# Kernel tuning notes

Measured on AMD Instinct MI355X. Metric: run time of the kernel, lower is better.

The kernel has to match this reference:

```python
import jax, jax.numpy as jnp
import numpy as np

LRELU = 0.2
EPS_LN = 1e-5
EPS_BN = 1e-5


def _seg_softmax(logits, seg, n):
    # softmax over edges grouped by destination node (PyG softmax), logits [E,H]
    m = jax.ops.segment_max(logits, seg, num_segments=n)
    e = jnp.exp(logits - m[seg])
    s = jax.ops.segment_sum(e, seg, num_segments=n)
    return e / (s[seg] + 1e-16)


def _gat(x, src, dst, n, W, a_src, a_dst, b, H, C):
    # PyG GATConv, concat=False (mean over heads), leaky_relu slope 0.2
    h = (x @ W).reshape(n, H, C)
    e = (h * a_src).sum(-1)[src] + (h * a_dst).sum(-1)[dst]  # [E,H]
    e = jnp.where(e > 0, e, LRELU * e)
    alpha = _seg_softmax(e, dst, n)
    out = jax.ops.segment_sum(h[src] * alpha[:, :, None], dst, num_segments=n)  # [N,H,C]
    return out.mean(1) + b


def _gcn(x, src, dst, n, W, b):
    # PyG GCNConv with symmetric normalization; edge list already contains self loops
    deg = jax.ops.segment_sum(jnp.ones(src.shape, x.dtype), dst, num_segments=n)
    dis = jnp.where(deg > 0, jax.lax.rsqrt(jnp.maximum(deg, 1e-12)), 0.0)
    h = x @ W
    w = (dis[src] * dis[dst])[:, None]
    return jax.ops.segment_sum(h[src] * w, dst, num_segments=n) + b


def _ln(x, g, b):
    mu = x.mean(-1, keepdims=True)
    v = x.var(-1, keepdims=True)
    return (x - mu) * jax.lax.rsqrt(v + EPS_LN) * g + b


def _bn_eval(x, g, b, rm, rv):
    return (x - rm) * jax.lax.rsqrt(rv + EPS_BN) * g + b


def _forward(x, edge_index, gin, bti, rmi, rvi, W1, as1, ad1, b1, Wg1, bg1,
             W2, as2, ad2, b2, Wg2, bg2, Ws, bs, Wf, bf,
             g1, be1, g2, be2, g3, be3, Wc1, bc1, gbn, bbn, rmb, rvb, Wc2, bc2):
    n = x.shape[0]
    xn = _bn_eval(x, gin, bti, rmi, rvi)
    sl = jnp.arange(n, dtype=edge_index.dtype)
    src = jnp.concatenate([edge_index[0], sl])
    dst = jnp.concatenate([edge_index[1], sl])
    # GAT1 (4 heads, 128) -> LN -> relu
    x1 = _gat(xn, src, dst, n, W1, as1, ad1, b1, 4, 128)
    x1 = jax.nn.relu(_ln(x1, g1, be1))
    # GCN1 -> relu
    x1g = jax.nn.relu(_gcn(x1, src, dst, n, Wg1, bg1))
    # GAT2 (2 heads, 64) -> LN -> relu
    x2 = _gat(x1g, src, dst, n, W2, as2, ad2, b2, 2, 64)
    x2 = jax.nn.relu(_ln(x2, g2, be2))
    # GCN2 -> relu
    x2g = jax.nn.relu(_gcn(x2, src, dst, n, Wg2, bg2))
    # skip + fusion
    skip = jax.nn.relu(xn @ Ws + bs)
    fused = jax.nn.relu(jnp.concatenate([x1g, x2g], axis=1) @ Wf + bf)
    final = _ln(fused + skip, g3, be3)
    # classifier: Linear -> BN(eval) -> relu -> Linear
    h = jax.nn.relu(_bn_eval(final @ Wc1 + bc1, gbn, bbn, rmb, rvb))
    return h @ Wc2 + bc2


def setup_inputs():
    key = jax.random.key(0)
    ks = jax.random.split(key, 20)
    N, F, E = 20000, 512, 160000
    H1, C1, H2, C2 = 4, 128, 2, 64
    rn = lambda k, sh, s=0.05: (jax.random.normal(k, sh) * s).astype(jnp.float32)
    return dict(
        x=jax.random.normal(ks[0], (N, F), jnp.float32),
        edge_index=jax.random.randint(ks[1], (2, E), 0, N, jnp.int32),
        gin=jnp.ones((F,), jnp.float32), bti=jnp.zeros((F,), jnp.float32),
        rmi=rn(ks[2], (F,)), rvi=(jax.random.uniform(ks[3], (F,)) + 0.5).astype(jnp.float32),
        W1=rn(ks[4], (F, H1 * C1)), as1=rn(ks[5], (H1, C1)), ad1=rn(ks[6], (H1, C1)), b1=jnp.zeros((C1,), jnp.float32),
        Wg1=rn(ks[7], (C1, C1)), bg1=jnp.zeros((C1,), jnp.float32),
        W2=rn(ks[8], (C1, H2 * C2)), as2=rn(ks[9], (H2, C2)), ad2=rn(ks[10], (H2, C2)), b2=jnp.zeros((C2,), jnp.float32),
        Wg2=rn(ks[11], (C2, C2)), bg2=jnp.zeros((C2,), jnp.float32),
        Ws=rn(ks[12], (F, C2)), bs=jnp.zeros((C2,), jnp.float32),
        Wf=rn(ks[13], (C1 + C2, C2)), bf=jnp.zeros((C2,), jnp.float32),
        g1=jnp.ones((C1,), jnp.float32), be1=jnp.zeros((C1,), jnp.float32),
        g2=jnp.ones((C2,), jnp.float32), be2=jnp.zeros((C2,), jnp.float32),
        g3=jnp.ones((C2,), jnp.float32), be3=jnp.zeros((C2,), jnp.float32),
        Wc1=rn(ks[14], (C2, 32)), bc1=jnp.zeros((32,), jnp.float32),
        gbn=jnp.ones((32,), jnp.float32), bbn=jnp.zeros((32,), jnp.float32),
        rmb=rn(ks[15], (32,)), rvb=(jax.random.uniform(ks[16], (32,)) + 0.5).astype(jnp.float32),
        Wc2=rn(ks[17], (32, 5)), bc2=jnp.zeros((5,), jnp.float32),
    )


def reference(x, edge_index, gin, bti, rmi, rvi, W1, as1, ad1, b1, Wg1, bg1,
              W2, as2, ad2, b2, Wg2, bg2, Ws, bs, Wf, bf,
              g1, be1, g2, be2, g3, be3, Wc1, bc1, gbn, bbn, rmb, rvb, Wc2, bc2):
    return _forward(x, edge_index, gin, bti, rmi, rvi, W1, as1, ad1, b1, Wg1, bg1,
                    W2, as2, ad2, b2, Wg2, bg2, Ws, bs, Wf, bf,
                    g1, be1, g2, be2, g3, be3, Wc1, bc1, gbn, bbn, rmb, rvb, Wc2, bc2)
```

## Files before the change

### kernel.cpp

```cpp
#include <hip/hip_runtime.h>
#include <hip/hip_bf16.h>

#define N_NODES 20000
#define F_IN 512

typedef __attribute__((ext_vector_type(8))) short short8;
typedef __attribute__((ext_vector_type(4))) float f32x4;

__device__ __forceinline__ ushort f2bf(float f) {
    uint u = __float_as_uint(f);
    u += 0x7FFF + ((u >> 16) & 1);
    return (ushort)(u >> 16);
}
__device__ __forceinline__ float bf2f(ushort h) { return __uint_as_float((uint)h << 16); }

__device__ __forceinline__ void gload_lds16(const void* g, void* l) {
    __builtin_amdgcn_global_load_lds(
        (const __attribute__((address_space(1))) void*)g,
        (__attribute__((address_space(3))) void*)l, 16, 0, 0);
}

__device__ __forceinline__ f32x4 shfl_xor4(f32x4 v, int m) {
    f32x4 r;
#pragma unroll
    for (int i = 0; i < 4; i++) r[i] = __shfl_xor(v[i], m);
    return r;
}

__global__ void zero_int_k(int* p, int n) {
    int i = blockIdx.x * blockDim.x + threadIdx.x;
    if (i < n) p[i] = 0;
}

__global__ void hist_k(const int* __restrict__ ei, int E0, int N, int* __restrict__ deg) {
    int e = blockIdx.x * blockDim.x + threadIdx.x;
    int Etot = E0 + N;
    if (e >= Etot) return;
    int dst = (e < E0) ? ei[E0 + e] : (e - E0);
    atomicAdd(&deg[dst], 1);
}

__global__ __launch_bounds__(1024) void scan_k(const int* __restrict__ deg, int* __restrict__ rp,
                                               int* __restrict__ fp, float* __restrict__ dis,
                                               int N, int Etot) {
    __shared__ int part[1024];
    int tid = threadIdx.x;
    int chunk = (N + 1023) / 1024;
    int lo = tid * chunk, hi = min(lo + chunk, N);
    int s = 0;
    for (int i = lo; i < hi; i++) s += deg[i];
    part[tid] = s;
    __syncthreads();
    for (int off = 1; off < 1024; off <<= 1) {
        int t = 0;
        if (tid >= off) t = part[tid - off];
        __syncthreads();
        part[tid] += t;
        __syncthreads();
    }
    int run = part[tid] - s;
    for (int i = lo; i < hi; i++) {
        rp[i] = run; fp[i] = run;
        int d = deg[i];
        dis[i] = (d > 0) ? rsqrtf((float)d) : 0.f;
        run += d;
    }
    if (tid == 1023) { rp[N] = Etot; fp[N] = Etot; }
}

__global__ void scatter_k(const int* __restrict__ ei, int E0, int N, int* __restrict__ fp,
                          int* __restrict__ csr_src) {
    int e = blockIdx.x * blockDim.x + threadIdx.x;
    int Etot = E0 + N;
    if (e >= Etot) return;
    int src, dst;
    if (e < E0) { src = ei[e]; dst = ei[E0 + e]; }
    else        { src = e - E0; dst = src; }
    int pos = atomicAdd(&fp[dst], 1);
    csr_src[pos] = src;
}

__global__ void bnprep_k(const float* __restrict__ g, const float* __restrict__ b,
                         const float* __restrict__ rm, const float* __restrict__ rv,
                         float* __restrict__ sc, float* __restrict__ sh, int n) {
    int i = blockIdx.x * blockDim.x + threadIdx.x;
    if (i >= n) return;
    float s = g[i] * rsqrtf(rv[i] + 1e-5f);
    sc[i] = s;
    sh[i] = b[i] - rm[i] * s;
}

__global__ void splitA_k(const float* __restrict__ x, const float* __restrict__ sc,
                         const float* __restrict__ sh, ushort* __restrict__ Ah,
                         ushort* __restrict__ Al, int M, int Mpad) {
    size_t i4 = (size_t)blockIdx.x * blockDim.x + threadIdx.x;
    size_t base = i4 * 4;
    if (base >= (size_t)Mpad * 512) return;
    int row = (int)(base >> 9);
    ushort4 ah = {0, 0, 0, 0}, al = {0, 0, 0, 0};
    if (row < M) {
        float4 v = *(const float4*)&x[base];
        int c = (int)(base & 511);
        float f0 = v.x * sc[c] + sh[c];
        float f1 = v.y * sc[c + 1] + sh[c + 1];
        float f2 = v.z * sc[c + 2] + sh[c + 2];
        float f3 = v.w * sc[c + 3] + sh[c + 3];
        ah.x = f2bf(f0); al.x = f2bf(f0 - bf2f(ah.x));
        ah.y = f2bf(f1); al.y = f2bf(f1 - bf2f(ah.y));
        ah.z = f2bf(f2); al.z = f2bf(f2 - bf2f(ah.z));
        ah.w = f2bf(f3); al.w = f2bf(f3 - bf2f(ah.w));
    }
    *(ushort4*)&Ah[base] = ah;
    *(ushort4*)&Al[base] = al;
}

__global__ __launch_bounds__(256) void splitBt_k(const float* __restrict__ W1, const float* __restrict__ Ws,
                                                 ushort* __restrict__ Bth, ushort* __restrict__ Btl) {
    __shared__ float tile[64][65];
    int n0 = blockIdx.x * 64;
    int k0 = blockIdx.y * 64;
    int t = threadIdx.x;
    int a = t >> 6, b = t & 63;
#pragma unroll
    for (int i = 0; i < 16; i++) {
        int kk = a + i * 4, nn = b;
        int gk = k0 + kk, gn = n0 + nn;
        float v;
        if (gn < 512)      v = W1[(size_t)gk * 512 + gn];
        else if (gn < 576) v = Ws[(size_t)gk * 64 + (gn - 512)];
        else               v = 0.f;
        tile[kk][nn] = v;
    }
    __syncthreads();
#pragma unroll
    for (int i = 0; i < 16; i++) {
        int nn = a + i * 4, kk = b;
        float v = tile[kk][nn];
        ushort hi = f2bf(v);
        ushort lo = f2bf(v - bf2f(hi));
        Bth[(size_t)(n0 + nn) * 512 + k0 + kk] = hi;
        Btl[(size_t)(n0 + nn) * 512 + k0 + kk] = lo;
    }
}

__global__ __launch_bounds__(256) void mfma_gemm_k(
    const ushort* __restrict__ Ah, const ushort* __restrict__ Al,
    const ushort* __restrict__ Bth, const ushort* __restrict__ Btl,
    const float* __restrict__ bs, const float* __restrict__ as1, const float* __restrict__ ad1,
    float* __restrict__ h1, float* __restrict__ skip,
    float* __restrict__ ss1, float* __restrict__ sd1,
    int M, int K) {
    __shared__ ushort A_s[128 * 64];
    __shared__ ushort B_s[128 * 64];
    __shared__ float s1buf[128], s2buf[128];
    int t = threadIdx.x;
    int w = t >> 6, l = t & 63;

    int nwg = gridDim.x;
    int q = nwg >> 3, r = nwg & 7;
    int xcd = blockIdx.x & 7, lid = blockIdx.x >> 3;
    int wg = (xcd < r) ? xcd * (q + 1) + lid : r * (q + 1) + (xcd - r) * q + lid;
    int by = wg / 5, bx = wg % 5;
    int bm = by * 128;
    int n0 = bx * 128;
    int r0 = (w & 1) * 64, c0 = (w >> 1) * 64;

    f32x4 acc[4][4] = {};

    int sl = (t & 7) ^ ((t >> 3) & 7);
    const ushort* aArr = (sl < 4) ? Ah : Al;
    const ushort* bArr = (sl < 4) ? Bth : Btl;
    int ko = (sl & 3) * 8;
    size_t asrc[4], bsrc[4];
#pragma unroll
    for (int c = 0; c < 4; c++) {
        int rr = c * 32 + (t >> 3);
        asrc[c] = (size_t)(bm + rr) * 512 + ko;
        bsrc[c] = (size_t)(n0 + rr) * 512 + ko;
    }
    int d0 = t * 8;

    for (int kt = 0; kt < K; kt += 32) {
#pragma unroll
        for (int c = 0; c < 4; c++) gload_lds16(aArr + asrc[c] + kt, &A_s[c * 2048 + d0]);
#pragma unroll
        for (int c = 0; c < 4; c++) gload_lds16(bArr + bsrc[c] + kt, &B_s[c * 2048 + d0]);
        __syncthreads();

        short8 ah[4], al4[4], bh[4], bl[4];
        int lr = l & 15, kg = l >> 4;
        int spa = kg ^ (lr & 7);
#pragma unroll
        for (int f = 0; f < 4; f++) {
            int ra = (r0 + f * 16 + lr) * 64;
            ah[f]  = *(const short8*)&A_s[ra + spa * 8];
            al4[f] = *(const short8*)&A_s[ra + (spa ^ 4) * 8];
            int rb = (c0 + f * 16 + lr) * 64;
            bh[f] = *(const short8*)&B_s[rb + spa * 8];
            bl[f] = *(const short8*)&B_s[rb + (spa ^ 4) * 8];
        }
#pragma unroll
        for (int fm = 0; fm < 4; fm++)
#pragma unroll
            for (int fn = 0; fn < 4; fn++) {
                acc[fm][fn] = __builtin_amdgcn_mfma_f32_16x16x32_bf16(ah[fm], bh[fn], acc[fm][fn], 0, 0, 0);
                acc[fm][fn] = __builtin_amdgcn_mfma_f32_16x16x32_bf16(ah[fm], bl[fn], acc[fm][fn], 0, 0, 0);
                acc[fm][fn] = __builtin_amdgcn_mfma_f32_16x16x32_bf16(al4[fm], bh[fn], acc[fm][fn], 0, 0, 0);
            }
        __syncthreads();
    }

    int lr = l & 15, kg = l >> 4;
#pragma unroll
    for (int fm = 0; fm < 4; fm++) {
        int row_base = bm + r0 + fm * 16 + kg * 4;
#pragma unroll
        for (int fn = 0; fn < 4; fn++) {
            int col = n0 + c0 + fn * 16 + lr;
#pragma unroll
            for (int r2 = 0; r2 < 4; r2++) {
                int row = row_base + r2;
                if (row < M) {
                    float v = acc[fm][fn][r2];
                    if (col < 512) h1[(size_t)row * 512 + col] = v;
                    else if (col < 576) skip[(size_t)row * 64 + (col - 512)] = fmaxf(v + bs[col - 512], 0.f);
                }
            }
        }
    }

    if (t < 128) { s1buf[t] = 0.f; s2buf[t] = 0.f; }
    __syncthreads();
    if (bx < 4) {
        float aw_[4], dw_[4];
#pragma unroll
        for (int fn = 0; fn < 4; fn++) {
            int col = n0 + c0 + fn * 16 + lr;
            aw_[fn] = as1[col];
            dw_[fn] = ad1[col];
        }
#pragma unroll
        for (int fm = 0; fm < 4; fm++)
#pragma unroll
            for (int r2 = 0; r2 < 4; r2++) {
                float p1 = acc[fm][0][r2] * aw_[0] + acc[fm][1][r2] * aw_[1] +
                           acc[fm][2][r2] * aw_[2] + acc[fm][3][r2] * aw_[3];
                float p2 = acc[fm][0][r2] * dw_[0] + acc[fm][1][r2] * dw_[1] +
                           acc[fm][2][r2] * dw_[2] + acc[fm][3][r2] * dw_[3];
#pragma unroll
                for (int off = 1; off < 16; off <<= 1) {
                    p1 += __shfl_xor(p1, off);
                    p2 += __shfl_xor(p2, off);
                }
                if (lr == 0) {
                    int rloc = r0 + fm * 16 + kg * 4 + r2;
                    atomicAdd(&s1buf[rloc], p1);
                    atomicAdd(&s2buf[rloc], p2);
                }
            }
    }
    __syncthreads();
    if (bx < 4 && t < 128 && bm + t < M) {
        ss1[(size_t)(bm + t) * 4 + bx] = s1buf[t];
        sd1[(size_t)(bm + t) * 4 + bx] = s2buf[t];
    }
}

template <int K, int NOUT, bool SC>
__global__ __launch_bounds__(NOUT) void rowgemm_k(const float* __restrict__ X, const float* __restrict__ W,
                                                  float* __restrict__ out,
                                                  const float* __restrict__ a_src, const float* __restrict__ a_dst,
                                                  float* __restrict__ ss, float* __restrict__ sd, int N) {
    __shared__ float Ws[K * NOUT];
    __shared__ float Xs[8][K];
    int c = threadIdx.x;
    for (int i = c; i < K * NOUT; i += NOUT) Ws[i] = W[i];
    float asv = 0.f, adv = 0.f;
    if (SC) { asv = a_src[c]; adv = a_dst[c]; }
    for (int r0 = blockIdx.x * 8; r0 < N; r0 += gridDim.x * 8) {
        int nr = min(8, N - r0);
        __syncthreads();
        for (int i = c; i < nr * K; i += NOUT) Xs[i / K][i % K] = X[(size_t)r0 * K + i];
        __syncthreads();
        float acc[8] = {};
        for (int k = 0; k < K; k++) {
            float w = Ws[k * NOUT + c];
#pragma unroll
            for (int r = 0; r < 8; r++) acc[r] += Xs[r][k] * w;
        }
        for (int r = 0; r < nr; r++) out[(size_t)(r0 + r) * NOUT + c] = acc[r];
        if (SC) {
            int head = c >> 6;
            for (int r = 0; r < nr; r++) {
                float p1 = acc[r] * asv, p2 = acc[r] * adv;
#pragma unroll
                for (int off = 1; off < 64; off <<= 1) {
                    p1 += __shfl_xor(p1, off);
                    p2 += __shfl_xor(p2, off);
                }
                if ((c & 63) == 0) {
                    ss[(size_t)(r0 + r) * 2 + head] = p1;
                    sd[(size_t)(r0 + r) * 2 + head] = p2;
                }
            }
        }
    }
}

template <int H, int C>
__global__ __launch_bounds__(C) void gat_agg_k(const float* __restrict__ h, const float* __restrict__ ss,
                                               const float* __restrict__ sd, const float* __restrict__ bias,
                                               const float* __restrict__ g, const float* __restrict__ be,
                                               const int* __restrict__ rp, const int* __restrict__ csr_src,
                                               float* __restrict__ out, int N) {
    int n = blockIdx.x;
    int tid = threadIdx.x;
    __shared__ float m_s[H], s_s[H];
    __shared__ __align__(16) float red4[32][4];
    __shared__ int srcs[64];
    __shared__ float aw[64 * H];
    int e0 = rp[n], deg = rp[n + 1] - e0;
    bool small = (deg <= 64);
    int hh = tid >> 5, l = tid & 31;

    if (small && tid < deg) srcs[tid] = csr_src[e0 + tid];
    __syncthreads();

    float sdv = sd[n * H + hh];
    float m = -1e30f, s = 0.f;
    for (int k = l; k < deg; k += 32) {
        int src = small ? srcs[k] : csr_src[e0 + k];
        float e = ss[src * H + hh] + sdv;
        e = (e > 0.f) ? e : 0.2f * e;
        if (small) aw[k * H + hh] = e;
        float mn = fmaxf(m, e);
        s = s * __expf(m - mn) + __expf(e - mn);
        m = mn;
    }
#pragma unroll
    for (int off = 16; off; off >>= 1) {
        float mo = __shfl_xor(m, off), so = __shfl_xor(s, off);
        float mn = fmaxf(m, mo);
        s = s * __expf(m - mn) + so * __expf(mo - mn);
        m = mn;
    }
    if (l == 0) { m_s[hh] = m; s_s[hh] = s + 1e-16f; }
    __syncthreads();

    constexpr int LPR = H * C / 4;
    constexpr int EIF = C / LPR;
    int ep = tid / LPR;
    int o  = (tid % LPR) * 4;
    int hq = o / C;
    f32x4 acc = {0.f, 0.f, 0.f, 0.f};

    if (small) {
        for (int idx = tid; idx < deg * H; idx += C) {
            int h2 = idx & (H - 1);
            aw[idx] = __expf(aw[idx] - m_s[h2]) / s_s[h2];
        }
        __syncthreads();
        for (int k = 0; k < deg; k += EIF) {
            int e = k + ep;
            if (EIF == 1 || e < deg) {
                f32x4 v = *(const f32x4*)(h + (size_t)srcs[e] * (H * C) + o);
                acc += aw[e * H + hq] * v;
            }
        }
    } else {
        for (int t0 = 0; t0 < deg; t0 += 64) {
            int tl = min(64, deg - t0);
            __syncthreads();
            if (tid < tl) srcs[tid] = csr_src[e0 + t0 + tid];
            __syncthreads();
            for (int idx = tid; idx < tl * H; idx += C) {
                int k = idx / H, h2 = idx & (H - 1);
                float e = ss[srcs[k] * H + h2] + sd[n * H + h2];
                e = (e > 0.f) ? e : 0.2f * e;
                aw[idx] = __expf(e - m_s[h2]) / s_s[h2];
            }
            __syncthreads();
            for (int k = 0; k < tl; k += EIF) {
                int e = k + ep;
                if (EIF == 1 || e < tl) {
                    f32x4 v = *(const f32x4*)(h + (size_t)srcs[e] * (H * C) + o);
                    acc += aw[e * H + hq] * v;
                }
            }
        }
    }

    if (H == 4) {
        acc += shfl_xor4(acc, 32);
        if (tid >= 64 && (tid & 63) < 32) *(f32x4*)&red4[tid & 31][0] = acc;
        __syncthreads();
        if (tid < 32) {
            f32x4 o2 = *(const f32x4*)&red4[tid][0];
            acc += o2;
            f32x4 b4 = *(const f32x4*)&bias[tid * 4];
            f32x4 v4 = acc * 0.25f + b4;
            float s1 = v4[0] + v4[1] + v4[2] + v4[3];
#pragma unroll
            for (int off = 1; off < 32; off <<= 1) s1 += __shfl_xor(s1, off);
            float mu = s1 * (1.f / C);
            f32x4 d4 = v4 - mu;
            float s2 = d4[0]*d4[0] + d4[1]*d4[1] + d4[2]*d4[2] + d4[3]*d4[3];
#pragma unroll
            for (int off = 1; off < 32; off <<= 1) s2 += __shfl_xor(s2, off);
            float rs = rsqrtf(s2 * (1.f / C) + 1e-5f);
            f32x4 g4 = *(const f32x4*)&g[tid * 4];
            f32x4 e4 = *(const f32x4*)&be[tid * 4];
            f32x4 y;
#pragma unroll
            for (int i = 0; i < 4; i++) y[i] = fmaxf(d4[i] * rs * g4[i] + e4[i], 0.f);
            *(f32x4*)(out + (size_t)n * C + tid * 4) = y;
        }
    } else {
        acc += shfl_xor4(acc, 32);
        acc += shfl_xor4(acc, 16);
        if (tid < 16) {
            f32x4 b4 = *(const f32x4*)&bias[tid * 4];
            f32x4 v4 = acc * 0.5f + b4;
            float s1 = v4[0] + v4[1] + v4[2] + v4[3];
#pragma unroll
            for (int off = 1; off < 16; off <<= 1) s1 += __shfl_xor(s1, off);
            float mu = s1 * (1.f / C);
            f32x4 d4 = v4 - mu;
            float s2 = d4[0]*d4[0] + d4[1]*d4[1] + d4[2]*d4[2] + d4[3]*d4[3];
#pragma unroll
            for (int off = 1; off < 16; off <<= 1) s2 += __shfl_xor(s2, off);
            float rs = rsqrtf(s2 * (1.f / C) + 1e-5f);
            f32x4 g4 = *(const f32x4*)&g[tid * 4];
            f32x4 e4 = *(const f32x4*)&be[tid * 4];
            f32x4 y;
#pragma unroll
            for (int i = 0; i < 4; i++) y[i] = fmaxf(d4[i] * rs * g4[i] + e4[i], 0.f);
            *(f32x4*)(out + (size_t)n * C + tid * 4) = y;
        }
    }
}

__global__ __launch_bounds__(128) void gcn_agg128_k(const float* __restrict__ h, const float* __restrict__ dis,
                                                    const float* __restrict__ bias, const int* __restrict__ rp,
                                                    const int* __restrict__ csr_src, float* __restrict__ out, int N) {
    int n = blockIdx.x;
    int tid = threadIdx.x;
    __shared__ int srcs[64];
    __shared__ float w[64];
    __shared__ __align__(16) float red4[32][4];
    int e0 = rp[n], deg = rp[n + 1] - e0;
    float dn = dis[n];
    int ep = tid >> 5;
    int c0 = (tid & 31) * 4;
    f32x4 acc = {0.f, 0.f, 0.f, 0.f};
    for (int t0 = 0; t0 < deg; t0 += 64) {
        int tl = min(64, deg - t0);
        if (tid < tl) {
            int s = csr_src[e0 + t0 + tid];
            srcs[tid] = s;
            w[tid] = dis[s] * dn;
        }
        __syncthreads();
        for (int k = 0; k < tl; k += 4) {
            int e = k + ep;
            if (e < tl) {
                f32x4 v = *(const f32x4*)(h + (size_t)srcs[e] * 128 + c0);
                acc += w[e] * v;
            }
        }
        __syncthreads();
    }
    acc += shfl_xor4(acc, 32);
    if (tid >= 64 && (tid & 63) < 32) *(f32x4*)&red4[tid & 31][0] = acc;
    __syncthreads();
    if (tid < 32) {
        f32x4 o2 = *(const f32x4*)&red4[tid][0];
        acc += o2;
        f32x4 b4 = *(const f32x4*)&bias[c0];
        f32x4 y;
#pragma unroll
        for (int i = 0; i < 4; i++) y[i] = fmaxf(acc[i] + b4[i], 0.f);
        *(f32x4*)(out + (size_t)n * 128 + c0) = y;
    }
}

__global__ __launch_bounds__(256) void final_fused_k(
    const float* __restrict__ hg2, const float* __restrict__ dis, const float* __restrict__ bg2,
    const int* __restrict__ rp, const int* __restrict__ csr_src,
    const float* __restrict__ x1g, const float* __restrict__ Wf, const float* __restrict__ bf,
    const float* __restrict__ skip, const float* __restrict__ g3, const float* __restrict__ be3,
    const float* __restrict__ Wc1, const float* __restrict__ bc1, const float* __restrict__ gbn,
    const float* __restrict__ bbn, const float* __restrict__ rmb, const float* __restrict__ rvb,
    const float* __restrict__ Wc2, const float* __restrict__ bc2, float* __restrict__ out, int N) {
    int wv = threadIdx.x >> 6;
    int t  = threadIdx.x & 63;
    int n = blockIdx.x * 4 + wv;
    __shared__ __align__(16) float cat_s[4][192];
    __shared__ float fbuf_s[4][64];
    __shared__ float hbuf_s[4][32];
    if (n >= N) return;

    int e0 = rp[n], deg = rp[n + 1] - e0;
    float dn = dis[n];
    int ep = t >> 4;
    int o = (t & 15) * 4;
    f32x4 acc = {0.f, 0.f, 0.f, 0.f};
    for (int k = 0; k < deg; k += 4) {
        int e = k + ep;
        if (e < deg) {
            int s = csr_src[e0 + e];
            f32x4 v = *(const f32x4*)(hg2 + (size_t)s * 64 + o);
            acc += (dis[s] * dn) * v;
        }
    }
    acc += shfl_xor4(acc, 32);
    acc += shfl_xor4(acc, 16);
    if (t < 16) {
        f32x4 b4 = *(const f32x4*)&bg2[t * 4];
        f32x4 xv;
#pragma unroll
        for (int i = 0; i < 4; i++) xv[i] = fmaxf(acc[i] + b4[i], 0.f);
        *(f32x4*)&cat_s[wv][128 + t * 4] = xv;
    }
    if (t < 32) *(f32x4*)&cat_s[wv][t * 4] = *(const f32x4*)(x1g + (size_t)n * 128 + t * 4);
    float fa = bf[t];
    const float* cat = cat_s[wv];
    for (int j = 0; j < 192; j++) fa += cat[j] * Wf[j * 64 + t];
    fa = fmaxf(fa, 0.f) + skip[(size_t)n * 64 + t];
    float t1 = fa;
#pragma unroll
    for (int off = 1; off < 64; off <<= 1) t1 += __shfl_xor(t1, off);
    float mu = t1 * (1.f / 64.f);
    float d = fa - mu;
    float t2 = d * d;
#pragma unroll
    for (int off = 1; off < 64; off <<= 1) t2 += __shfl_xor(t2, off);
    float var = t2 * (1.f / 64.f);
    fbuf_s[wv][t] = d * rsqrtf(var + 1e-5f) * g3[t] + be3[t];
    if (t < 32) {
        float a = bc1[t];
        for (int j = 0; j < 64; j++) a += fbuf_s[wv][j] * Wc1[j * 32 + t];
        a = (a - rmb[t]) * rsqrtf(rvb[t] + 1e-5f) * gbn[t] + bbn[t];
        hbuf_s[wv][t] = fmaxf(a, 0.f);
    }
    if (t < 5) {
        float a = bc2[t];
        for (int j = 0; j < 32; j++) a += hbuf_s[wv][j] * Wc2[j * 5 + t];
        out[(size_t)n * 5 + t] = a;
    }
}

extern "C" void kernel_launch(void* const* d_in, const int* in_sizes, int n_in,
                              void* d_out, int out_size, void* d_ws, size_t ws_size,
                              hipStream_t stream) {
    const float* x   = (const float*)d_in[0];
    const int*   ei  = (const int*)d_in[1];
    const float* gin = (const float*)d_in[2];
    const float* bti = (const float*)d_in[3];
    const float* rmi = (const float*)d_in[4];
    const float* rvi = (const float*)d_in[5];
    const float* W1  = (const float*)d_in[6];
    const float* as1 = (const float*)d_in[7];
    const float* ad1 = (const float*)d_in[8];
    const float* b1  = (const float*)d_in[9];
    const float* Wg1 = (const float*)d_in[10];
    const float* bg1 = (const float*)d_in[11];
    const float* W2  = (const float*)d_in[12];
    const float* as2 = (const float*)d_in[13];
    const float* ad2 = (const float*)d_in[14];
    const float* b2  = (const float*)d_in[15];
    const float* Wg2 = (const float*)d_in[16];
    const float* bg2 = (const float*)d_in[17];
    const float* Ws  = (const float*)d_in[18];
    const float* bs  = (const float*)d_in[19];
    const float* Wf  = (const float*)d_in[20];
    const float* bf  = (const float*)d_in[21];
    const float* g1  = (const float*)d_in[22];
    const float* be1 = (const float*)d_in[23];
    const float* g2  = (const float*)d_in[24];
    const float* be2 = (const float*)d_in[25];
    const float* g3  = (const float*)d_in[26];
    const float* be3 = (const float*)d_in[27];
    const float* Wc1 = (const float*)d_in[28];
    const float* bc1 = (const float*)d_in[29];
    const float* gbn = (const float*)d_in[30];
    const float* bbn = (const float*)d_in[31];
    const float* rmb = (const float*)d_in[32];
    const float* rvb = (const float*)d_in[33];
    const float* Wc2 = (const float*)d_in[34];
    const float* bc2 = (const float*)d_in[35];
    float* out = (float*)d_out;

    const int N = in_sizes[0] / F_IN;
    const int E0 = in_sizes[1] / 2;
    const int Etot = E0 + N;
    const int Mpad = 20096;

    char* wp = (char*)d_ws;
    auto alloc = [&](size_t bytes) -> void* {
        void* p = (void*)wp;
        wp += (bytes + 255) & ~(size_t)255;
        return p;
    };
    float* h1   = (float*)alloc((size_t)N * 512 * 4);
    ushort* Ah  = (ushort*)alloc((size_t)Mpad * 512 * 2);
    ushort* Al  = (ushort*)alloc((size_t)Mpad * 512 * 2);
    ushort* Bth = (ushort*)alloc((size_t)640 * 512 * 2);
    ushort* Btl = (ushort*)alloc((size_t)640 * 512 * 2);
    float* skip = (float*)alloc((size_t)N * 64 * 4);
    float* ss1  = (float*)alloc((size_t)N * 4 * 4);
    float* sd1  = (float*)alloc((size_t)N * 4 * 4);
    float* ss2  = (float*)alloc((size_t)N * 2 * 4);
    float* sd2  = (float*)alloc((size_t)N * 2 * 4);
    float* dis  = (float*)alloc((size_t)N * 4);
    float* sc   = (float*)alloc((size_t)F_IN * 4);
    float* sh   = (float*)alloc((size_t)F_IN * 4);
    int* deg    = (int*)alloc((size_t)N * 4);
    int* rp     = (int*)alloc((size_t)(N + 1) * 4);
    int* fp     = (int*)alloc((size_t)(N + 1) * 4);
    int* csr    = (int*)alloc((size_t)Etot * 4);
    float* hg1 = h1;
    float* x1g = h1 + (size_t)N * 128;
    float* h2  = h1 + (size_t)N * 256;
    float* x2  = h1 + (size_t)N * 384;
    float* hg2 = h1 + (size_t)N * 448;
    float* x1  = (float*)Ah;

    zero_int_k<<<(N + 255) / 256, 256, 0, stream>>>(deg, N);
    hist_k<<<(Etot + 255) / 256, 256, 0, stream>>>(ei, E0, N, deg);
    scan_k<<<1, 1024, 0, stream>>>(deg, rp, fp, dis, N, Etot);
    scatter_k<<<(Etot + 255) / 256, 256, 0, stream>>>(ei, E0, N, fp, csr);
    bnprep_k<<<2, 256, 0, stream>>>(gin, bti, rmi, rvi, sc, sh, F_IN);
    splitA_k<<<(int)(((size_t)Mpad * 512 / 4 + 255) / 256), 256, 0, stream>>>(x, sc, sh, Ah, Al, N, Mpad);
    splitBt_k<<<dim3(10, 8), 256, 0, stream>>>(W1, Ws, Bth, Btl);

    mfma_gemm_k<<<785, 256, 0, stream>>>(Ah, Al, Bth, Btl, bs, as1, ad1, h1, skip, ss1, sd1, N, 512);

    gat_agg_k<4, 128><<<N, 128, 0, stream>>>(h1, ss1, sd1, b1, g1, be1, rp, csr, x1, N);

    rowgemm_k<128, 128, false><<<1280, 128, 0, stream>>>(x1, Wg1, hg1, nullptr, nullptr, nullptr, nullptr, N);
    gcn_agg128_k<<<N, 128, 0, stream>>>(hg1, dis, bg1, rp, csr, x1g, N);

    rowgemm_k<128, 128, true><<<1280, 128, 0, stream>>>(x1g, W2, h2, as2, ad2, ss2, sd2, N);
    gat_agg_k<2, 64><<<N, 64, 0, stream>>>(h2, ss2, sd2, b2, g2, be2, rp, csr, x2, N);

    rowgemm_k<64, 64, false><<<1280, 64, 0, stream>>>(x2, Wg2, hg2, nullptr, nullptr, nullptr, nullptr, N);

    final_fused_k<<<(N + 3) / 4, 256, 0, stream>>>(hg2, dis, bg2, rp, csr, x1g, Wf, bf, skip, g3, be3,
                                                   Wc1, bc1, gbn, bbn, rmb, rvb, Wc2, bc2, out, N);
}
```

Baseline: 555.5 us.

## Fuse graph aggregation stages with following dense GEMMs into per-tile kernels

Replaces the separate GAT aggregation, GCN aggregation and row-GEMM kernels with three fused kernels. Each block aggregates 8 nodes (one wave per two nodes) into shared memory and then multiplies them by the next layer's weight matrix. This removes the global round-trips and launches for the intermediate x1/x2 activations. Weights are now read from global/L2 per block rather than staged in LDS. GAT1 aggregation processes one node per wave with per-edge recompute of alpha instead of block-wide edge staging.

```diff
diff --git a/kernel.cpp b/kernel.cpp
--- a/kernel.cpp
+++ b/kernel.cpp
@@ -266,221 +266,246 @@
     }
 }
 
-template <int K, int NOUT, bool SC>
-__global__ __launch_bounds__(NOUT) void rowgemm_k(const float* __restrict__ X, const float* __restrict__ W,
-                                                  float* __restrict__ out,
-                                                  const float* __restrict__ a_src, const float* __restrict__ a_dst,
-                                                  float* __restrict__ ss, float* __restrict__ sd, int N) {
-    __shared__ float Ws[K * NOUT];
-    __shared__ float Xs[8][K];
-    int c = threadIdx.x;
-    for (int i = c; i < K * NOUT; i += NOUT) Ws[i] = W[i];
-    float asv = 0.f, adv = 0.f;
-    if (SC) { asv = a_src[c]; adv = a_dst[c]; }
-    for (int r0 = blockIdx.x * 8; r0 < N; r0 += gridDim.x * 8) {
-        int nr = min(8, N - r0);
-        __syncthreads();
-        for (int i = c; i < nr * K; i += NOUT) Xs[i / K][i % K] = X[(size_t)r0 * K + i];
-        __syncthreads();
-        float acc[8] = {};
-        for (int k = 0; k < K; k++) {
-            float w = Ws[k * NOUT + c];
-#pragma unroll
-            for (int r = 0; r < 8; r++) acc[r] += Xs[r][k] * w;
-        }
-        for (int r = 0; r < nr; r++) out[(size_t)(r0 + r) * NOUT + c] = acc[r];
-        if (SC) {
-            int head = c >> 6;
-            for (int r = 0; r < nr; r++) {
-                float p1 = acc[r] * asv, p2 = acc[r] * adv;
-#pragma unroll
-                for (int off = 1; off < 64; off <<= 1) {
-                    p1 += __shfl_xor(p1, off);
-                    p2 += __shfl_xor(p2, off);
+__global__ __launch_bounds__(256) void gat1_gcn1_k(
+    const float* __restrict__ h1, const float* __restrict__ ss1, const float* __restrict__ sd1,
+    const float* __restrict__ b1, const float* __restrict__ g1, const float* __restrict__ be1,
+    const int* __restrict__ rp, const int* __restrict__ csr,
+    const float* __restrict__ Wg1, float* __restrict__ hg1, int N) {
+    __shared__ __align__(16) float x1s[8][128];
+    int t = threadIdx.x;
+    int l = t & 63, wv = t >> 6;
+    int hh = l >> 4, lr = l & 15;
+
+    for (int i = 0; i < 2; i++) {
+        int nl = wv * 2 + i;
+        int n = blockIdx.x * 8 + nl;
+        if (n < N) {
+            int e0 = rp[n], deg = rp[n + 1] - e0;
+            float sdv = sd1[n * 4 + hh];
+            float m = -1e30f, s = 0.f;
+            for (int k = lr; k < deg; k += 16) {
+                int src = csr[e0 + k];
+                float e = ss1[src * 4 + hh] + sdv;
+                e = (e > 0.f) ? e : 0.2f * e;
+                float mn = fmaxf(m, e);
+                s = s * __expf(m - mn) + __expf(e - mn);
+                m = mn;
+            }
+#pragma unroll
+            for (int off = 8; off; off >>= 1) {
+                float mo = __shfl_xor(m, off), so = __shfl_xor(s, off);
+                float mn = fmaxf(m, mo);
+                s = s * __expf(m - mn) + so * __expf(mo - mn);
+                m = mn;
+            }
+            s += 1e-16f;
+            f32x4 a0 = {0, 0, 0, 0}, a1 = {0, 0, 0, 0};
+            for (int k = 0; k < deg; k++) {
+                int src = csr[e0 + k];
+                float e = ss1[src * 4 + hh] + sdv;
+                e = (e > 0.f) ? e : 0.2f * e;
+                float al = __expf(e - m) / s;
+                const float* hp = h1 + (size_t)src * 512 + hh * 128 + lr * 8;
+                a0 += al * *(const f32x4*)hp;
+                a1 += al * *(const f32x4*)(hp + 4);
+            }
+            a0 += shfl_xor4(a0, 16); a1 += shfl_xor4(a1, 16);
+            a0 += shfl_xor4(a0, 32); a1 += shfl_xor4(a1, 32);
+            f32x4 v0 = a0 * 0.25f + *(const f32x4*)&b1[lr * 8];
+            f32x4 v1 = a1 * 0.25f + *(const f32x4*)&b1[lr * 8 + 4];
+            float s1 = v0[0] + v0[1] + v0[2] + v0[3] + v1[0] + v1[1] + v1[2] + v1[3];
+#pragma unroll
+            for (int off = 8; off; off >>= 1) s1 += __shfl_xor(s1, off);
+            float mu = s1 * (1.f / 128.f);
+            f32x4 d0 = v0 - mu, d1 = v1 - mu;
+            float s2 = d0[0]*d0[0] + d0[1]*d0[1] + d0[2]*d0[2] + d0[3]*d0[3] +
+                       d1[0]*d1[0] + d1[1]*d1[1] + d1[2]*d1[2] + d1[3]*d1[3];
+#pragma unroll
+            for (int off = 8; off; off >>= 1) s2 += __shfl_xor(s2, off);
+            float rs = rsqrtf(s2 * (1.f / 128.f) + 1e-5f);
+            if (l < 16) {
+                f32x4 g4a = *(const f32x4*)&g1[lr * 8], g4b = *(const f32x4*)&g1[lr * 8 + 4];
+                f32x4 e4a = *(const f32x4*)&be1[lr * 8], e4b = *(const f32x4*)&be1[lr * 8 + 4];
+                f32x4 y0, y1;
+#pragma unroll
+                for (int j = 0; j < 4; j++) {
+                    y0[j] = fmaxf(d0[j] * rs * g4a[j] + e4a[j], 0.f);
+                    y1[j] = fmaxf(d1[j] * rs * g4b[j] + e4b[j], 0.f);
                 }
-                if ((c & 63) == 0) {
-                    ss[(size_t)(r0 + r) * 2 + head] = p1;
-                    sd[(size_t)(r0 + r) * 2 + head] = p2;
-                }
-            }
-        }
-    }
-}
-
-template <int H, int C>
-__global__ __launch_bounds__(C) void gat_agg_k(const float* __restrict__ h, const float* __restrict__ ss,
-                                               const float* __restrict__ sd, const float* __restrict__ bias,
-                                               const float* __restrict__ g, const float* __restrict__ be,
-                                               const int* __restrict__ rp, const int* __restrict__ csr_src,
-                                               float* __restrict__ out, int N) {
-    int n = blockIdx.x;
-    int tid = threadIdx.x;
-    __shared__ float m_s[H], s_s[H];
-    __shared__ __align__(16) float red4[32][4];
-    __shared__ int srcs[64];
-    __shared__ float aw[64 * H];
-    int e0 = rp[n], deg = rp[n + 1] - e0;
-    bool small = (deg <= 64);
-    int hh = tid >> 5, l = tid & 31;
-
-    if (small && tid < deg) srcs[tid] = csr_src[e0 + tid];
+                *(f32x4*)&x1s[nl][lr * 8] = y0;
+                *(f32x4*)&x1s[nl][lr * 8 + 4] = y1;
+            }
+        }
+    }
     __syncthreads();
 
-    float sdv = sd[n * H + hh];
-    float m = -1e30f, s = 0.f;
-    for (int k = l; k < deg; k += 32) {
-        int src = small ? srcs[k] : csr_src[e0 + k];
-        float e = ss[src * H + hh] + sdv;
-        e = (e > 0.f) ? e : 0.2f * e;
-        if (small) aw[k * H + hh] = e;
-        float mn = fmaxf(m, e);
-        s = s * __expf(m - mn) + __expf(e - mn);
-        m = mn;
-    }
-#pragma unroll
-    for (int off = 16; off; off >>= 1) {
-        float mo = __shfl_xor(m, off), so = __shfl_xor(s, off);
-        float mn = fmaxf(m, mo);
-        s = s * __expf(m - mn) + so * __expf(mo - mn);
-        m = mn;
-    }
-    if (l == 0) { m_s[hh] = m; s_s[hh] = s + 1e-16f; }
+    int c = t & 127, rh = t >> 7;
+    float acc[4] = {};
+    for (int k = 0; k < 128; k += 4) {
+        float w0 = Wg1[(size_t)k * 128 + c];
+        float w1 = Wg1[(size_t)(k + 1) * 128 + c];
+        float w2 = Wg1[(size_t)(k + 2) * 128 + c];
+        float w3 = Wg1[(size_t)(k + 3) * 128 + c];
+#pragma unroll
+        for (int r = 0; r < 4; r++) {
+            f32x4 xv = *(const f32x4*)&x1s[rh * 4 + r][k];
+            acc[r] += xv[0] * w0 + xv[1] * w1 + xv[2] * w2 + xv[3] * w3;
+        }
+    }
+    for (int r = 0; r < 4; r++) {
+        int n = blockIdx.x * 8 + rh * 4 + r;
+        if (n < N) hg1[(size_t)n * 128 + c] = acc[r];
+    }
+}
+
+__global__ __launch_bounds__(256) void gcn1_gat2gemm_k(
+    const float* __restrict__ hg1, const float* __restrict__ dis, const float* __restrict__ bg1,
+    const int* __restrict__ rp, const int* __restrict__ csr,
+    const float* __restrict__ W2, const float* __restrict__ as2, const float* __restrict__ ad2,
+    float* __restrict__ x1g, float* __restrict__ h2,
+    float* __restrict__ ss2, float* __restrict__ sd2, int N) {
+    __shared__ __align__(16) float xs[8][128];
+    int t = threadIdx.x;
+    int l = t & 63, wv = t >> 6;
+    int ep = l >> 5, c4 = (l & 31) * 4;
+
+    for (int i = 0; i < 2; i++) {
+        int nl = wv * 2 + i;
+        int n = blockIdx.x * 8 + nl;
+        if (n < N) {
+            int e0 = rp[n], deg = rp[n + 1] - e0;
+            float dn = dis[n];
+            f32x4 acc = {0, 0, 0, 0};
+            for (int k = ep; k < deg; k += 2) {
+                int src = csr[e0 + k];
+                acc += (dis[src] * dn) * *(const f32x4*)(hg1 + (size_t)src * 128 + c4);
+            }
+            acc += shfl_xor4(acc, 32);
+            if (l < 32) {
+                f32x4 b4 = *(const f32x4*)&bg1[c4];
+                f32x4 y;
+#pragma unroll
+                for (int j = 0; j < 4; j++) y[j] = fmaxf(acc[j] + b4[j], 0.f);
+                *(f32x4*)&xs[nl][c4] = y;
+                *(f32x4*)(x1g + (size_t)n * 128 + c4) = y;
+            }
+        }
+    }
     __syncthreads();
 
-    constexpr int LPR = H * C / 4;
-    constexpr int EIF = C / LPR;
-    int ep = tid / LPR;
-    int o  = (tid % LPR) * 4;
-    int hq = o / C;
-    f32x4 acc = {0.f, 0.f, 0.f, 0.f};
-
-    if (small) {
-        for (int idx = tid; idx < deg * H; idx += C) {
-            int h2 = idx & (H - 1);
-            aw[idx] = __expf(aw[idx] - m_s[h2]) / s_s[h2];
-        }
-        __syncthreads();
-        for (int k = 0; k < deg; k += EIF) {
-            int e = k + ep;
-            if (EIF == 1 || e < deg) {
-                f32x4 v = *(const f32x4*)(h + (size_t)srcs[e] * (H * C) + o);
-                acc += aw[e * H + hq] * v;
-            }
-        }
-    } else {
-        for (int t0 = 0; t0 < deg; t0 += 64) {
-            int tl = min(64, deg - t0);
-            __syncthreads();
-            if (tid < tl) srcs[tid] = csr_src[e0 + t0 + tid];
-            __syncthreads();
-            for (int idx = tid; idx < tl * H; idx += C) {
-                int k = idx / H, h2 = idx & (H - 1);
-                float e = ss[srcs[k] * H + h2] + sd[n * H + h2];
+    int c = t & 127, rh = t >> 7;
+    int head = (t >> 6) & 1;
+    float asv = as2[c], adv = ad2[c];
+    float acc[4] = {};
+    for (int k = 0; k < 128; k += 4) {
+        float w0 = W2[(size_t)k * 128 + c];
+        float w1 = W2[(size_t)(k + 1) * 128 + c];
+        float w2 = W2[(size_t)(k + 2) * 128 + c];
+        float w3 = W2[(size_t)(k + 3) * 128 + c];
+#pragma unroll
+        for (int r = 0; r < 4; r++) {
+            f32x4 xv = *(const f32x4*)&xs[rh * 4 + r][k];
+            acc[r] += xv[0] * w0 + xv[1] * w1 + xv[2] * w2 + xv[3] * w3;
+        }
+    }
+    for (int r = 0; r < 4; r++) {
+        int n = blockIdx.x * 8 + rh * 4 + r;
+        if (n < N) h2[(size_t)n * 128 + c] = acc[r];
+        float p1 = acc[r] * asv, p2 = acc[r] * adv;
+#pragma unroll
+        for (int off = 1; off < 64; off <<= 1) {
+            p1 += __shfl_xor(p1, off);
+            p2 += __shfl_xor(p2, off);
+        }
+        if (l == 0 && n < N) {
+            ss2[(size_t)n * 2 + head] = p1;
+            sd2[(size_t)n * 2 + head] = p2;
+        }
+    }
+}
+
+__global__ __launch_bounds__(256) void gat2_gcn2gemm_k(
+    const float* __restrict__ h2, const float* __restrict__ ss2, const float* __restrict__ sd2,
+    const float* __restrict__ b2, const float* __restrict__ g2, const float* __restrict__ be2,
+    const int* __restrict__ rp, const int* __restrict__ csr,
+    const float* __restrict__ Wg2, float* __restrict__ hg2, int N) {
+    __shared__ __align__(16) float xs[8][64];
+    int t = threadIdx.x;
+    int l = t & 63, wv = t >> 6;
+    int hh = l >> 5, lr = l & 31, c2 = lr * 2;
+
+    for (int i = 0; i < 2; i++) {
+        int nl = wv * 2 + i;
+        int n = blockIdx.x * 8 + nl;
+        if (n < N) {
+            int e0 = rp[n], deg = rp[n + 1] - e0;
+            float sdv = sd2[n * 2 + hh];
+            float m = -1e30f, s = 0.f;
+            for (int k = lr; k < deg; k += 32) {
+                int src = csr[e0 + k];
+                float e = ss2[src * 2 + hh] + sdv;
                 e = (e > 0.f) ? e : 0.2f * e;
-                aw[idx] = __expf(e - m_s[h2]) / s_s[h2];
-            }
-            __syncthreads();
-            for (int k = 0; k < tl; k += EIF) {
-                int e = k + ep;
-                if (EIF == 1 || e < tl) {
-                    f32x4 v = *(const f32x4*)(h + (size_t)srcs[e] * (H * C) + o);
-                    acc += aw[e * H + hq] * v;
-                }
-            }
-        }
-    }
-
-    if (H == 4) {
-        acc += shfl_xor4(acc, 32);
-        if (tid >= 64 && (tid & 63) < 32) *(f32x4*)&red4[tid & 31][0] = acc;
-        __syncthreads();
-        if (tid < 32) {
-            f32x4 o2 = *(const f32x4*)&red4[tid][0];
-            acc += o2;
-            f32x4 b4 = *(const f32x4*)&bias[tid * 4];
-            f32x4 v4 = acc * 0.25f + b4;
-            float s1 = v4[0] + v4[1] + v4[2] + v4[3];
-#pragma unroll
-            for (int off = 1; off < 32; off <<= 1) s1 += __shfl_xor(s1, off);
-            float mu = s1 * (1.f / C);
-            f32x4 d4 = v4 - mu;
-            float s2 = d4[0]*d4[0] + d4[1]*d4[1] + d4[2]*d4[2] + d4[3]*d4[3];
-#pragma unroll
-            for (int off = 1; off < 32; off <<= 1) s2 += __shfl_xor(s2, off);
-            float rs = rsqrtf(s2 * (1.f / C) + 1e-5f);
-            f32x4 g4 = *(const f32x4*)&g[tid * 4];
-            f32x4 e4 = *(const f32x4*)&be[tid * 4];
-            f32x4 y;
-#pragma unroll
-            for (int i = 0; i < 4; i++) y[i] = fmaxf(d4[i] * rs * g4[i] + e4[i], 0.f);
-            *(f32x4*)(out + (size_t)n * C + tid * 4) = y;
-        }
-    } else {
-        acc += shfl_xor4(acc, 32);
-        acc += shfl_xor4(acc, 16);
-        if (tid < 16) {
-            f32x4 b4 = *(const f32x4*)&bias[tid * 4];
-            f32x4 v4 = acc * 0.5f + b4;
-            float s1 = v4[0] + v4[1] + v4[2] + v4[3];
-#pragma unroll
-            for (int off = 1; off < 16; off <<= 1) s1 += __shfl_xor(s1, off);
-            float mu = s1 * (1.f / C);
-            f32x4 d4 = v4 - mu;
-            float s2 = d4[0]*d4[0] + d4[1]*d4[1] + d4[2]*d4[2] + d4[3]*d4[3];
-#pragma unroll
-            for (int off = 1; off < 16; off <<= 1) s2 += __shfl_xor(s2, off);
-            float rs = rsqrtf(s2 * (1.f / C) + 1e-5f);
-            f32x4 g4 = *(const f32x4*)&g[tid * 4];
-            f32x4 e4 = *(const f32x4*)&be[tid * 4];
-            f32x4 y;
-#pragma unroll
-            for (int i = 0; i < 4; i++) y[i] = fmaxf(d4[i] * rs * g4[i] + e4[i], 0.f);
-            *(f32x4*)(out + (size_t)n * C + tid * 4) = y;
-        }
-    }
-}
-
-__global__ __launch_bounds__(128) void gcn_agg128_k(const float* __restrict__ h, const float* __restrict__ dis,
-                                                    const float* __restrict__ bias, const int* __restrict__ rp,
-                                                    const int* __restrict__ csr_src, float* __restrict__ out, int N) {
-    int n = blockIdx.x;
-    int tid = threadIdx.x;
-    __shared__ int srcs[64];
-    __shared__ float w[64];
-    __shared__ __align__(16) float red4[32][4];
-    int e0 = rp[n], deg = rp[n + 1] - e0;
-    float dn = dis[n];
-    int ep = tid >> 5;
-    int c0 = (tid & 31) * 4;
-    f32x4 acc = {0.f, 0.f, 0.f, 0.f};
-    for (int t0 = 0; t0 < deg; t0 += 64) {
-        int tl = min(64, deg - t0);
-        if (tid < tl) {
-            int s = csr_src[e0 + t0 + tid];
-            srcs[tid] = s;
-            w[tid] = dis[s] * dn;
-        }
-        __syncthreads();
-        for (int k = 0; k < tl; k += 4) {
-            int e = k + ep;
-            if (e < tl) {
-                f32x4 v = *(const f32x4*)(h + (size_t)srcs[e] * 128 + c0);
-                acc += w[e] * v;
-            }
-        }
-        __syncthreads();
-    }
-    acc += shfl_xor4(acc, 32);
-    if (tid >= 64 && (tid & 63) < 32) *(f32x4*)&red4[tid & 31][0] = acc;
+                float mn = fmaxf(m, e);
+                s = s * __expf(m - mn) + __expf(e - mn);
+                m = mn;
+            }
+#pragma unroll
+            for (int off = 16; off; off >>= 1) {
+                float mo = __shfl_xor(m, off), so = __shfl_xor(s, off);
+                float mn = fmaxf(m, mo);
+                s = s * __expf(m - mn) + so * __expf(mo - mn);
+                m = mn;
+            }
+            s += 1e-16f;
+            float a0 = 0.f, a1 = 0.f;
+            for (int k = 0; k < deg; k++) {
+                int src = csr[e0 + k];
+                float e = ss2[src * 2 + hh] + sdv;
+                e = (e > 0.f) ? e : 0.2f * e;
+                float al = __expf(e - m) / s;
+                const float* hp = h2 + (size_t)src * 128 + hh * 64 + c2;
+                a0 += al * hp[0];
+                a1 += al * hp[1];
+            }
+            a0 += __shfl_xor(a0, 32);
+            a1 += __shfl_xor(a1, 32);
+            float v0 = a0 * 0.5f + b2[c2];
+            float v1 = a1 * 0.5f + b2[c2 + 1];
+            float s1 = v0 + v1;
+#pragma unroll
+            for (int off = 16; off; off >>= 1) s1 += __shfl_xor(s1, off);
+            float mu = s1 * (1.f / 64.f);
+            float d0 = v0 - mu, d1 = v1 - mu;
+            float s2 = d0 * d0 + d1 * d1;
+#pragma unroll
+            for (int off = 16; off; off >>= 1) s2 += __shfl_xor(s2, off);
+            float rs = rsqrtf(s2 * (1.f / 64.f) + 1e-5f);
+            if (l < 32) {
+                float y0 = fmaxf(d0 * rs * g2[c2] + be2[c2], 0.f);
+                float y1 = fmaxf(d1 * rs * g2[c2 + 1] + be2[c2 + 1], 0.f);
+                float2 y = {y0, y1};
+                *(float2*)&xs[nl][c2] = y;
+            }
+        }
+    }
     __syncthreads();
-    if (tid < 32) {
-        f32x4 o2 = *(const f32x4*)&red4[tid][0];
-        acc += o2;
-        f32x4 b4 = *(const f32x4*)&bias[c0];
-        f32x4 y;
-#pragma unroll
-        for (int i = 0; i < 4; i++) y[i] = fmaxf(acc[i] + b4[i], 0.f);
-        *(f32x4*)(out + (size_t)n * 128 + c0) = y;
+
+    int c = t & 63, rg = t >> 6;
+    float acc[2] = {};
+    for (int k = 0; k < 64; k += 4) {
+        float w0 = Wg2[(size_t)k * 64 + c];
+        float w1 = Wg2[(size_t)(k + 1) * 64 + c];
+        float w2 = Wg2[(size_t)(k + 2) * 64 + c];
+        float w3 = Wg2[(size_t)(k + 3) * 64 + c];
+#pragma unroll
+        for (int r = 0; r < 2; r++) {
+            f32x4 xv = *(const f32x4*)&xs[rg * 2 + r][k];
+            acc[r] += xv[0] * w0 + xv[1] * w1 + xv[2] * w2 + xv[3] * w3;
+        }
+    }
+    for (int r = 0; r < 2; r++) {
+        int n = blockIdx.x * 8 + rg * 2 + r;
+        if (n < N) hg2[(size_t)n * 64 + c] = acc[r];
     }
 }
 
@@ -502,25 +527,21 @@
 
     int e0 = rp[n], deg = rp[n + 1] - e0;
     float dn = dis[n];
-    int ep = t >> 4;
-    int o = (t & 15) * 4;
-    f32x4 acc = {0.f, 0.f, 0.f, 0.f};
-    for (int k = 0; k < deg; k += 4) {
-        int e = k + ep;
-        if (e < deg) {
-            int s = csr_src[e0 + e];
-            f32x4 v = *(const f32x4*)(hg2 + (size_t)s * 64 + o);
-            acc += (dis[s] * dn) * v;
-        }
+    int ep = t >> 4, o = (t & 15) * 4;
+    f32x4 acc = {0, 0, 0, 0};
+    for (int k = ep; k < deg; k += 4) {
+        int s = csr_src[e0 + k];
+        f32x4 v = *(const f32x4*)(hg2 + (size_t)s * 64 + o);
+        acc += (dis[s] * dn) * v;
     }
     acc += shfl_xor4(acc, 32);
     acc += shfl_xor4(acc, 16);
     if (t < 16) {
-        f32x4 b4 = *(const f32x4*)&bg2[t * 4];
+        f32x4 b4 = *(const f32x4*)&bg2[o];
         f32x4 xv;
 #pragma unroll
         for (int i = 0; i < 4; i++) xv[i] = fmaxf(acc[i] + b4[i], 0.f);
-        *(f32x4*)&cat_s[wv][128 + t * 4] = xv;
+        *(f32x4*)&cat_s[wv][128 + o] = xv;
     }
     if (t < 32) *(f32x4*)&cat_s[wv][t * 4] = *(const f32x4*)(x1g + (size_t)n * 128 + t * 4);
     float fa = bf[t];
@@ -619,12 +640,10 @@
     int* rp     = (int*)alloc((size_t)(N + 1) * 4);
     int* fp     = (int*)alloc((size_t)(N + 1) * 4);
     int* csr    = (int*)alloc((size_t)Etot * 4);
-    float* hg1 = h1;
-    float* x1g = h1 + (size_t)N * 128;
-    float* h2  = h1 + (size_t)N * 256;
-    float* x2  = h1 + (size_t)N * 384;
-    float* hg2 = h1 + (size_t)N * 448;
-    float* x1  = (float*)Ah;
+    float* hg1 = (float*)Ah;
+    float* x1g = hg1 + (size_t)N * 128;
+    float* h2  = hg1 + (size_t)N * 256;
+    float* hg2 = hg1 + (size_t)N * 384;
 
     zero_int_k<<<(N + 255) / 256, 256, 0, stream>>>(deg, N);
     hist_k<<<(Etot + 255) / 256, 256, 0, stream>>>(ei, E0, N, deg);
@@ -636,16 +655,10 @@
 
     mfma_gemm_k<<<785, 256, 0, stream>>>(Ah, Al, Bth, Btl, bs, as1, ad1, h1, skip, ss1, sd1, N, 512);
 
-    gat_agg_k<4, 128><<<N, 128, 0, stream>>>(h1, ss1, sd1, b1, g1, be1, rp, csr, x1, N);
-
-    rowgemm_k<128, 128, false><<<1280, 128, 0, stream>>>(x1, Wg1, hg1, nullptr, nullptr, nullptr, nullptr, N);
-    gcn_agg128_k<<<N, 128, 0, stream>>>(hg1, dis, bg1, rp, csr, x1g, N);
-
-    rowgemm_k<128, 128, true><<<1280, 128, 0, stream>>>(x1g, W2, h2, as2, ad2, ss2, sd2, N);
-    gat_agg_k<2, 64><<<N, 64, 0, stream>>>(h2, ss2, sd2, b2, g2, be2, rp, csr, x2, N);
-
-    rowgemm_k<64, 64, false><<<1280, 64, 0, stream>>>(x2, Wg2, hg2, nullptr, nullptr, nullptr, nullptr, N);
-
+    gat1_gcn1_k<<<(N + 7) / 8, 256, 0, stream>>>(h1, ss1, sd1, b1, g1, be1, rp, csr, Wg1, hg1, N);
+    gcn1_gat2gemm_k<<<(N + 7) / 8, 256, 0, stream>>>(hg1, dis, bg1, rp, csr, W2, as2, ad2,
+                                                     x1g, h2, ss2, sd2, N);
+    gat2_gcn2gemm_k<<<(N + 7) / 8, 256, 0, stream>>>(h2, ss2, sd2, b2, g2, be2, rp, csr, Wg2, hg2, N);
     final_fused_k<<<(N + 3) / 4, 256, 0, stream>>>(hg2, dis, bg2, rp, csr, x1g, Wf, bf, skip, g3, be3,
                                                    Wc1, bc1, gbn, bbn, rmb, rvb, Wc2, bc2, out, N);
 }
```

After: 722.7 us. 30.1% more time.
